# Kernel tuning notes

Measured on AMD Instinct MI355X. Metric: run time of the kernel, lower is better.

## Reference

```python
import jax, jax.numpy as jnp
import numpy as np
from jax import lax

STRIDE = 2  # down_sample_stride
MATMUL_NORM = True


def maxpool2d_5d(x, s):
    # x: [B, T, C, H, W]; kernel=s, stride=s, padding=(s-1)//2 == 0 for s=2
    return lax.reduce_window(
        x, -jnp.inf, lax.max,
        window_dimensions=(1, 1, 1, s, s),
        window_strides=(1, 1, 1, s, s),
        padding='VALID')


def setup_inputs() -> dict:
    key = jax.random.key(0)
    k1, k2, k3, k4 = jax.random.split(key, 4)
    B, T, Ck, Cv, H, W = 2, 4, 64, 256, 64, 64
    return {
        'memory_keys': jax.random.normal(k1, (B, T, Ck, H, W), jnp.float32),
        'memory_values': jax.random.normal(k2, (B, T, Cv, H, W), jnp.float32),
        'query_key': jax.random.normal(k3, (B, Ck, H, W), jnp.float32),
        'query_value': jax.random.normal(k4, (B, Cv, H, W), jnp.float32),
    }


def reference(memory_keys, memory_values, query_key, query_value):
    B, T, Ck, oH, oW = memory_keys.shape
    Cv = memory_values.shape[2]
    # down-sample memory bank (max pool, stride 2, no padding)
    mk = maxpool2d_5d(memory_keys, STRIDE)   # [B,T,Ck,h,w]
    mv = maxpool2d_5d(memory_values, STRIDE) # [B,T,Cv,h,w]
    h, w = mk.shape[-2], mk.shape[-1]
    M = T * h * w
    N = oH * oH  # code uses ori_height*ori_height (square assumed)
    # permute(0,2,1,3,4).view(B,Ck,M).permute(0,2,1) -> [B, M, Ck]
    mk = mk.transpose(0, 2, 1, 3, 4).reshape(B, Ck, M).transpose(0, 2, 1)
    qk = query_key.reshape(B, Ck, N)
    attn = jnp.einsum('bmc,bcn->bmn', mk, qk)  # [B, M, N]
    if MATMUL_NORM:
        attn = attn * (Ck ** -0.5)
    attn = jax.nn.softmax(attn, axis=1)  # softmax over memory positions
    mv = mv.transpose(0, 2, 1, 3, 4).reshape(B, Cv, M)
    memory = jnp.einsum('bcm,bmn->bcn', mv, attn).reshape(B, Cv, oH, oW)
    return jnp.concatenate([query_value, memory], axis=1)  # [B, 2*Cv, H, W]
```

## Files before the change

kernel.cpp:

```cpp
#include <hip/hip_runtime.h>
#include <hip/hip_bf16.h>
#include <math.h>

typedef unsigned short u16;
typedef unsigned int   u32;
typedef __attribute__((ext_vector_type(8))) short  bf16x8;
typedef __attribute__((ext_vector_type(4))) float  floatx4;

#define NB 2
#define NT 4
#define CK 64
#define CV 256
#define HH 64
#define WW 64
#define MM 4096
#define NN 4096
#define SCALE 0.125f
#define SHIFT 4.0f
#define OUT_B 2097152
#define NW 64
#define ITG 16
#define C1 0.18033688011112042f
#define C2 (-5.770780163555853f)

__device__ __forceinline__ u16 f2b(float f) {
    __hip_bfloat16 h = __float2bfloat16(f);
    union { __hip_bfloat16 h; u16 u; } v; v.h = h; return v.u;
}

#define PRE_K 65536
#define PRE_V 589824
#define PRE_T 1114112

__global__ void prep(const float* __restrict__ mk, const float* __restrict__ mv,
                     const float4* __restrict__ qv,
                     u16* __restrict__ pk2, u16* __restrict__ vt,
                     float* __restrict__ out) {
    int u = blockIdx.x * 256 + threadIdx.x;
    if (u < PRE_K) {
        int m = u & 4095, cb8 = (u >> 12) & 7, b = u >> 15;
        int t = m >> 10, hh = (m >> 5) & 31, ww = m & 31;
        const float* s0 = mk + ((size_t)((b*NT + t)*CK + cb8*8))*(HH*WW)
                             + (2*hh)*WW + 2*ww;
        bf16x8 fr;
        #pragma unroll
        for (int i = 0; i < 8; ++i) {
            const float* s = s0 + (size_t)i*(HH*WW);
            float2 r0 = *(const float2*)s;
            float2 r1 = *(const float2*)(s + WW);
            fr[i] = (short)f2b(fmaxf(fmaxf(r0.x, r0.y), fmaxf(r1.x, r1.y)));
        }
        *(bf16x8*)(pk2 + ((size_t)(b*8 + cb8)*MM + m)*8) = fr;
    } else if (u < PRE_V) {
        int u2 = u - PRE_K;
        int m4 = u2 & 1023, c = (u2 >> 10) & 255, b = u2 >> 18;
        int t = m4 >> 8, hh = (m4 >> 3) & 31, w8 = m4 & 7;
        const float* s0 = mv + ((size_t)((b*NT + t)*CV + c))*(HH*WW)
                             + (2*hh)*WW + 8*w8;
        float4 a0 = *(const float4*)(s0);
        float4 a1 = *(const float4*)(s0 + 4);
        float4 b0 = *(const float4*)(s0 + WW);
        float4 b1 = *(const float4*)(s0 + WW + 4);
        ushort4 r;
        r.x = f2b(fmaxf(fmaxf(a0.x, a0.y), fmaxf(b0.x, b0.y)));
        r.y = f2b(fmaxf(fmaxf(a0.z, a0.w), fmaxf(b0.z, b0.w)));
        r.z = f2b(fmaxf(fmaxf(a1.x, a1.y), fmaxf(b1.x, b1.y)));
        r.w = f2b(fmaxf(fmaxf(a1.z, a1.w), fmaxf(b1.z, b1.w)));
        *(ushort4*)(vt + ((size_t)(b*CV + c)*MM) + m4*4) = r;
    } else {
        int u3 = u - PRE_V;
        int b = u3 >> 18, ru = u3 & 262143;
        ((float4*)out)[(size_t)b*(OUT_B/4) + ru] = qv[u3];
    }
}

__device__ __forceinline__ void qk_phase(bf16x8 k0, bf16x8 k1,
        const bf16x8 (&qf)[2][4], float (&sacc)[4],
        u16* __restrict__ Pd, int lrow, int cbw, int sw)
{
    #pragma unroll
    for (int t = 0; t < 4; ++t) {
        floatx4 s = __builtin_amdgcn_mfma_f32_16x16x32_bf16(
                        k0, qf[0][t], (floatx4){0.f,0.f,0.f,0.f}, 0, 0, 0);
        s = __builtin_amdgcn_mfma_f32_16x16x32_bf16(k1, qf[1][t], s, 0, 0, 0);
        float p0 = exp2f(__builtin_fmaf(s[0], C1, C2));
        float p1 = exp2f(__builtin_fmaf(s[1], C1, C2));
        float p2 = exp2f(__builtin_fmaf(s[2], C1, C2));
        float p3 = exp2f(__builtin_fmaf(s[3], C1, C2));
        sacc[t] += (p0 + p1) + (p2 + p3);
        u32 d0 = (u32)f2b(p0) | ((u32)f2b(p1) << 16);
        u32 d1 = (u32)f2b(p2) | ((u32)f2b(p3) << 16);
        *(uint2*)&Pd[(t*16 + lrow)*128 + ((cbw ^ sw) << 2)] = make_uint2(d0, d1);
    }
}

__device__ __forceinline__ void pv_phase(const bf16x8 (&vf)[4],
        floatx4 (&oacc)[4], const u16* __restrict__ Ps,
        int lrow, int quad, int sw)
{
    #pragma unroll
    for (int cc = 0; cc < 4; ++cc) {
        bf16x8 pf[4];
        #pragma unroll
        for (int t = 0; t < 4; ++t) {
            int cb = (cc << 3) + (quad << 1);
            pf[t] = *(const bf16x8*)&Ps[(t*16 + lrow)*128 + ((cb ^ sw) << 2)];
        }
        __builtin_amdgcn_s_setprio(1);
        #pragma unroll
        for (int t = 0; t < 4; ++t)
            oacc[t] = __builtin_amdgcn_mfma_f32_16x16x32_bf16(
                          vf[cc], pf[t], oacc[t], 0, 0, 0);
        __builtin_amdgcn_s_setprio(0);
    }
}

__launch_bounds__(512, 4)
__global__ void attn_v8(const u16* __restrict__ pk2, const u16* __restrict__ vt,
                        const float* __restrict__ qk,
                        float* __restrict__ part, float* __restrict__ sums) {
    const int bid = blockIdx.x;
    const int xcd = bid & 7;
    const int b  = (xcd >> 2) & 1;
    const int cs = (xcd >> 1) & 1;
    const int ms = xcd & 1;
    const int ntile = bid >> 3;
    const int tid = threadIdx.x, w = tid >> 6, l = tid & 63;
    const int lrow = l & 15, quad = l >> 4;
    const int n0 = ntile * NW;
    const int sw  = lrow << 1;
    const int cbw = (w << 2) + quad;
    const int mstart = ms << 11;

    __shared__ __align__(16) u16 P[2][NW * 128];
    __shared__ float sums_s[8][NW];

    bf16x8 qf[2][4];
    const float* qb = qk + (size_t)b * CK * NN + n0;
    #pragma unroll
    for (int cc = 0; cc < 2; ++cc)
        #pragma unroll
        for (int t = 0; t < 4; ++t)
            #pragma unroll
            for (int i = 0; i < 8; ++i) {
                int c = cc*32 + quad*8 + i;
                qf[cc][t][i] = (short)f2b(qb[(size_t)c*NN + t*16 + lrow]);
            }

    const u16* pkb  = pk2 + (size_t)b * (8*MM*8);
    const int  mrw  = mstart + w*16 + lrow;
    const u16* vrow = vt + ((size_t)b*CV + cs*128 + w*16 + lrow)*MM
                         + mstart + quad*8;

    floatx4 oacc[4];
    #pragma unroll
    for (int t = 0; t < 4; ++t) oacc[t] = (floatx4){0.f, 0.f, 0.f, 0.f};
    float sacc[4] = {0.f, 0.f, 0.f, 0.f};

    bf16x8 k0 = *(const bf16x8*)(pkb + ((size_t)quad*MM + mrw)*8);
    bf16x8 k1 = *(const bf16x8*)(pkb + ((size_t)(quad+4)*MM + mrw)*8);
    bf16x8 vf[4];
    #pragma unroll
    for (int cc = 0; cc < 4; ++cc)
        vf[cc] = *(const bf16x8*)(vrow + cc*32);
    qk_phase(k0, k1, qf, sacc, P[0], lrow, cbw, sw);

    for (int it = 0; it < ITG - 1; ++it) {
        __syncthreads();
        const int mb2 = (it + 1) << 7;
        bf16x8 k0n = *(const bf16x8*)(pkb + ((size_t)quad*MM + mb2 + mrw)*8);
        bf16x8 k1n = *(const bf16x8*)(pkb + ((size_t)(quad+4)*MM + mb2 + mrw)*8);
        bf16x8 vn[4];
        #pragma unroll
        for (int cc = 0; cc < 4; ++cc)
            vn[cc] = *(const bf16x8*)(vrow + mb2 + cc*32);
        pv_phase(vf, oacc, P[it & 1], lrow, quad, sw);
        qk_phase(k0n, k1n, qf, sacc, P[(it + 1) & 1], lrow, cbw, sw);
        #pragma unroll
        for (int cc = 0; cc < 4; ++cc) vf[cc] = vn[cc];
    }
    __syncthreads();
    pv_phase(vf, oacc, P[(ITG - 1) & 1], lrow, quad, sw);

    #pragma unroll
    for (int t = 0; t < 4; ++t) {
        float v = sacc[t];
        v += __shfl_xor(v, 16, 64);
        v += __shfl_xor(v, 32, 64);
        if (l < 16) sums_s[w][t*16 + l] = v;
    }
    __syncthreads();

    float* pb = part + ((size_t)((((ms*NB + b)*2 + cs)*64) + ntile)) * (128*64);
    #pragma unroll
    for (int t = 0; t < 4; ++t)
        #pragma unroll
        for (int r = 0; r < 4; ++r) {
            int c_loc = w*16 + quad*4 + r;
            pb[c_loc*64 + t*16 + lrow] = oacc[t][r];
        }
    if (cs == 0 && tid < 64) {
        float sv = 0.f;
        #pragma unroll
        for (int w2 = 0; w2 < 8; ++w2) sv += sums_s[w2][tid];
        sums[((size_t)((ms*NB + b)*64 + ntile))*64 + tid] = sv;
    }
}

__global__ void epilogue2(const float* __restrict__ part,
                          const float* __restrict__ sums,
                          float* __restrict__ out) {
    int e = blockIdx.x * 256 + threadIdx.x;
    int nl4 = e & 15;
    int nt  = (e >> 4) & 63;
    int c   = (e >> 10) & 255;
    int b   = e >> 18;
    int cs = c >> 7, cl = c & 127;
    const float4* p4 = (const float4*)part;
    const float4* s4 = (const float4*)sums;
    size_t t0 = (size_t)(((0*NB + b)*2 + cs)*64 + nt);
    size_t t1 = (size_t)(((1*NB + b)*2 + cs)*64 + nt);
    float4 u0 = p4[t0*2048 + cl*16 + nl4];
    float4 u1 = p4[t1*2048 + cl*16 + nl4];
    float4 d0 = s4[((size_t)((0*NB + b)*64 + nt))*16 + nl4];
    float4 d1 = s4[((size_t)((1*NB + b)*64 + nt))*16 + nl4];
    float4 r;
    r.x = (u0.x + u1.x) / (d0.x + d1.x);
    r.y = (u0.y + u1.y) / (d0.y + d1.y);
    r.z = (u0.z + u1.z) / (d0.z + d1.z);
    r.w = (u0.w + u1.w) / (d0.w + d1.w);
    ((float4*)out)[(size_t)(b*512 + 256 + c)*1024 + nt*16 + nl4] = r;
}


__global__ void pool_v_f32(const float* __restrict__ src, float* __restrict__ out) {
    int e = blockIdx.x * 256 + threadIdx.x;
    int c = e & 255;
    int r = e >> 8;
    int ww = r & 31;  int hh = (r >> 5) & 31;
    int t  = (r >> 10) & 3;  int b = r >> 12;
    int m  = r & (MM - 1);
    const float* s = src + ((size_t)(((b*NT + t)*CV + c)*HH + 2*hh))*WW + 2*ww;
    out[(size_t)b*OUT_B + (size_t)m*CV + c] = fmaxf(fmaxf(s[0], s[1]), fmaxf(s[WW], s[WW+1]));
}

__global__ void pool_k_f32(const float* __restrict__ src, float* __restrict__ dst) {
    int e = blockIdx.x * 256 + threadIdx.x;
    int c = e & 63;
    int r = e >> 6;
    int ww = r & 31;  int hh = (r >> 5) & 31;
    int t  = (r >> 10) & 3;  int b = r >> 12;
    const float* s = src + ((size_t)(((b*NT + t)*CK + c)*HH + 2*hh))*WW + 2*ww;
    dst[e] = fmaxf(fmaxf(s[0], s[1]), fmaxf(s[WW], s[WW+1]));
}

__global__ void copy_qv_f32(const float4* __restrict__ src, float4* __restrict__ dst) {
    int u = blockIdx.x * 256 + threadIdx.x;
    int b  = u >> 18;
    int ru = u & 262143;
    dst[(size_t)b * (OUT_B/4) + ru] = src[u];
}

template<bool STAGED_K>
__launch_bounds__(256)
__global__ void attn_old(const float* __restrict__ pk,
                         const float* __restrict__ mk,
                         const float* __restrict__ qk,
                         float* __restrict__ out) {
    __shared__ __align__(16) float q_lds[CK][4];
    __shared__ __align__(16) float sarr[4][MM];
    __shared__ float inv_l[4];

    const int tid = threadIdx.x;
    const int blk = blockIdx.x;
    const int b   = blk >> 10;
    const int n0  = (blk & 1023) << 2;

    {
        int c = tid >> 2, qi = tid & 3;
        q_lds[c][qi] = qk[((size_t)(b*CK + c))*NN + n0 + qi];
    }
    __syncthreads();

    #pragma unroll
    for (int i = 0; i < 16; ++i) {
        int m = tid + (i << 8);
        float a0 = 0.f, a1 = 0.f, a2 = 0.f, a3 = 0.f;
        if (STAGED_K) {
            const float4* k4 = reinterpret_cast<const float4*>(pk + ((size_t)b*MM + m)*CK);
            #pragma unroll
            for (int cc = 0; cc < 16; ++cc) {
                float4 kv = k4[cc];
                int c = cc*4;
                float4 q0 = *reinterpret_cast<const float4*>(&q_lds[c][0]);
                float4 q1 = *reinterpret_cast<const float4*>(&q_lds[c+1][0]);
                float4 q2 = *reinterpret_cast<const float4*>(&q_lds[c+2][0]);
                float4 q3 = *reinterpret_cast<const float4*>(&q_lds[c+3][0]);
                a0 += kv.x*q0.x + kv.y*q1.x + kv.z*q2.x + kv.w*q3.x;
                a1 += kv.x*q0.y + kv.y*q1.y + kv.z*q2.y + kv.w*q3.y;
                a2 += kv.x*q0.z + kv.y*q1.z + kv.z*q2.z + kv.w*q3.z;
                a3 += kv.x*q0.w + kv.y*q1.w + kv.z*q2.w + kv.w*q3.w;
            }
        } else {
            int ww = m & 31, hh = (m >> 5) & 31, t = m >> 10;
            const float* base = mk + ((size_t)((b*NT + t)*CK)*HH + 2*hh)*WW + 2*ww;
            for (int c = 0; c < CK; ++c) {
                const float* s = base + (size_t)c*HH*WW;
                float kv = fmaxf(fmaxf(s[0], s[1]), fmaxf(s[WW], s[WW+1]));
                float4 q = *reinterpret_cast<const float4*>(&q_lds[c][0]);
                a0 += kv*q.x; a1 += kv*q.y; a2 += kv*q.z; a3 += kv*q.w;
            }
        }
        sarr[0][m] = a0*SCALE;
        sarr[1][m] = a1*SCALE;
        sarr[2][m] = a2*SCALE;
        sarr[3][m] = a3*SCALE;
    }
    __syncthreads();

    const int wave = tid >> 6, lane = tid & 63;
    float mx = -3.0e38f;
    for (int m = lane; m < MM; m += 64) mx = fmaxf(mx, sarr[wave][m]);
    #pragma unroll
    for (int off = 32; off > 0; off >>= 1) mx = fmaxf(mx, __shfl_xor(mx, off, 64));
    float ls = 0.f;
    for (int m = lane; m < MM; m += 64) {
        float p = __expf(sarr[wave][m] - mx);
        sarr[wave][m] = p;
        ls += p;
    }
    #pragma unroll
    for (int off = 32; off > 0; off >>= 1) ls += __shfl_xor(ls, off, 64);
    if (lane == 0) inv_l[wave] = 1.0f / ls;
    __syncthreads();

    const int c4 = lane;
    const float4* vb = reinterpret_cast<const float4*>(out + (size_t)b*OUT_B) + c4;
    const float* prow = sarr[wave];
    float a0 = 0.f, a1 = 0.f, a2 = 0.f, a3 = 0.f;
    for (int m = 0; m < MM; m += 4) {
        float4 p4 = *reinterpret_cast<const float4*>(prow + m);
        const float4* vp = vb + (size_t)m*(CV/4);
        float4 v0 = vp[0], v1 = vp[CV/4], v2 = vp[CV/2], v3 = vp[3*(CV/4)];
        a0 += p4.x*v0.x + p4.y*v1.x + p4.z*v2.x + p4.w*v3.x;
        a1 += p4.x*v0.y + p4.y*v1.y + p4.z*v2.y + p4.w*v3.y;
        a2 += p4.x*v0.z + p4.y*v1.z + p4.z*v2.z + p4.w*v3.z;
        a3 += p4.x*v0.w + p4.y*v1.w + p4.z*v2.w + p4.w*v3.w;
    }

    float inv = inv_l[wave];
    int n = n0 + wave;
    size_t ob = ((size_t)(b*512 + 256 + c4*4))*NN + n;
    out[ob]        = a0*inv;
    out[ob + NN]   = a1*inv;
    out[ob + 2*NN] = a2*inv;
    out[ob + 3*NN] = a3*inv;
}


extern "C" void kernel_launch(void* const* d_in, const int* in_sizes, int n_in,
                              void* d_out, int out_size, void* d_ws, size_t ws_size,
                              hipStream_t stream) {
    const float* mk = (const float*)d_in[0];
    const float* mv = (const float*)d_in[1];
    const float* qk = (const float*)d_in[2];
    const float* qv = (const float*)d_in[3];
    float* out = (float*)d_out;

    u16* pk2 = (u16*)d_ws;
    u16* vt  = pk2 + (size_t)NB*8*MM*8;
    float* part = (float*)(vt + (size_t)NB*CV*MM);
    float* sums = part + 4194304;
    const size_t need = ((size_t)NB*8*MM*8 + (size_t)NB*CV*MM) * sizeof(u16)
                      + (4194304 + 16384) * sizeof(float);

    if (ws_size >= need) {
        prep<<<PRE_T/256, 256, 0, stream>>>(mk, mv, (const float4*)qv, pk2, vt, out);
        attn_v8<<<512, 512, 0, stream>>>(pk2, vt, qk, part, sums);
        epilogue2<<<524288/256, 256, 0, stream>>>(part, sums, out);
    } else {
        const size_t pk_bytes = (size_t)NB*MM*CK*sizeof(float);
        const bool staged = (ws_size >= pk_bytes);
        float* pk = (float*)d_ws;
        pool_v_f32<<<(NB*MM*CV)/256, 256, 0, stream>>>(mv, out);
        if (staged) {
            pool_k_f32<<<(NB*MM*CK)/256, 256, 0, stream>>>(mk, pk);
            attn_old<true ><<<NB*(NN/4), 256, 0, stream>>>(pk, mk, qk, out);
        } else {
            attn_old<false><<<NB*(NN/4), 256, 0, stream>>>(pk, mk, qk, out);
        }
        copy_qv_f32<<<((NB*CV*HH*WW)/4)/256, 256, 0, stream>>>((const float4*)qv, (float4*)out);
    }
}
```

Baseline: 143.4 us.

## Merge Cv halves per block so QK softmax is computed once, use raw exp/cvt asm

Each block now covers all 256 value channels (two 16-row tiles per wave) instead of splitting Cv into two halves across blocks. This stops the QK^T scores and exponentials from being computed twice, and the grid shrinks from 512 to 256 blocks. The exp2 call and the bf16 packing are replaced with inline v_exp_f32 and v_cvt_pk_bf16_f32 to cut VALU work. The trade-offs are higher register pressure (launch bounds drop to 2 blocks per CU) and fewer blocks for occupancy.

```diff
diff --git a/kernel.cpp b/kernel.cpp
--- a/kernel.cpp
+++ b/kernel.cpp
@@ -26,6 +26,17 @@
 __device__ __forceinline__ u16 f2b(float f) {
     __hip_bfloat16 h = __float2bfloat16(f);
     union { __hip_bfloat16 h; u16 u; } v; v.h = h; return v.u;
+}
+
+__device__ __forceinline__ float fexp2(float x) {
+    float r;
+    asm("v_exp_f32 %0, %1" : "=v"(r) : "v"(x));
+    return r;
+}
+__device__ __forceinline__ u32 cvtpk_bf16(float a, float b) {
+    u32 r;
+    asm("v_cvt_pk_bf16_f32 %0, %1, %2" : "=v"(r) : "v"(a), "v"(b));
+    return r;
 }
 
 #define PRE_K 65536
@@ -83,48 +94,46 @@
         floatx4 s = __builtin_amdgcn_mfma_f32_16x16x32_bf16(
                         k0, qf[0][t], (floatx4){0.f,0.f,0.f,0.f}, 0, 0, 0);
         s = __builtin_amdgcn_mfma_f32_16x16x32_bf16(k1, qf[1][t], s, 0, 0, 0);
-        float p0 = exp2f(__builtin_fmaf(s[0], C1, C2));
-        float p1 = exp2f(__builtin_fmaf(s[1], C1, C2));
-        float p2 = exp2f(__builtin_fmaf(s[2], C1, C2));
-        float p3 = exp2f(__builtin_fmaf(s[3], C1, C2));
+        float p0 = fexp2(__builtin_fmaf(s[0], C1, C2));
+        float p1 = fexp2(__builtin_fmaf(s[1], C1, C2));
+        float p2 = fexp2(__builtin_fmaf(s[2], C1, C2));
+        float p3 = fexp2(__builtin_fmaf(s[3], C1, C2));
         sacc[t] += (p0 + p1) + (p2 + p3);
-        u32 d0 = (u32)f2b(p0) | ((u32)f2b(p1) << 16);
-        u32 d1 = (u32)f2b(p2) | ((u32)f2b(p3) << 16);
+        u32 d0 = cvtpk_bf16(p0, p1);
+        u32 d1 = cvtpk_bf16(p2, p3);
         *(uint2*)&Pd[(t*16 + lrow)*128 + ((cbw ^ sw) << 2)] = make_uint2(d0, d1);
     }
 }
 
-__device__ __forceinline__ void pv_phase(const bf16x8 (&vf)[4],
-        floatx4 (&oacc)[4], const u16* __restrict__ Ps,
+__device__ __forceinline__ void pv_phase(const bf16x8 (&vf)[4][2],
+        floatx4 (&oacc)[2][4], const u16* __restrict__ Ps,
         int lrow, int quad, int sw)
 {
     #pragma unroll
-    for (int cc = 0; cc < 4; ++cc) {
-        bf16x8 pf[4];
-        #pragma unroll
-        for (int t = 0; t < 4; ++t) {
-            int cb = (cc << 3) + (quad << 1);
-            pf[t] = *(const bf16x8*)&Ps[(t*16 + lrow)*128 + ((cb ^ sw) << 2)];
+    for (int kt = 0; kt < 4; ++kt) {
+        int cb = (kt << 3) + (quad << 1);
+        #pragma unroll
+        for (int nt = 0; nt < 4; ++nt) {
+            bf16x8 pf = *(const bf16x8*)&Ps[(nt*16 + lrow)*128 + ((cb ^ sw) << 2)];
+            __builtin_amdgcn_s_setprio(1);
+            oacc[0][nt] = __builtin_amdgcn_mfma_f32_16x16x32_bf16(
+                              vf[kt][0], pf, oacc[0][nt], 0, 0, 0);
+            oacc[1][nt] = __builtin_amdgcn_mfma_f32_16x16x32_bf16(
+                              vf[kt][1], pf, oacc[1][nt], 0, 0, 0);
+            __builtin_amdgcn_s_setprio(0);
         }
-        __builtin_amdgcn_s_setprio(1);
-        #pragma unroll
-        for (int t = 0; t < 4; ++t)
-            oacc[t] = __builtin_amdgcn_mfma_f32_16x16x32_bf16(
-                          vf[cc], pf[t], oacc[t], 0, 0, 0);
-        __builtin_amdgcn_s_setprio(0);
-    }
-}
-
-__launch_bounds__(512, 4)
-__global__ void attn_v8(const u16* __restrict__ pk2, const u16* __restrict__ vt,
-                        const float* __restrict__ qk,
-                        float* __restrict__ part, float* __restrict__ sums) {
+    }
+}
+
+__launch_bounds__(512, 2)
+__global__ void attn_v10(const u16* __restrict__ pk2, const u16* __restrict__ vt,
+                         const float* __restrict__ qk,
+                         float* __restrict__ part, float* __restrict__ sums) {
     const int bid = blockIdx.x;
-    const int xcd = bid & 7;
-    const int b  = (xcd >> 2) & 1;
-    const int cs = (xcd >> 1) & 1;
-    const int ms = xcd & 1;
-    const int ntile = bid >> 3;
+    const int xcd = bid & 7, grp = bid >> 3;
+    const int b   = (xcd >> 2) & 1;
+    const int ms  = xcd & 1;
+    const int ntile = (((xcd >> 1) & 1) << 5) | grp;
     const int tid = threadIdx.x, w = tid >> 6, l = tid & 63;
     const int lrow = l & 15, quad = l >> 4;
     const int n0 = ntile * NW;
@@ -149,20 +158,24 @@
 
     const u16* pkb  = pk2 + (size_t)b * (8*MM*8);
     const int  mrw  = mstart + w*16 + lrow;
-    const u16* vrow = vt + ((size_t)b*CV + cs*128 + w*16 + lrow)*MM
-                         + mstart + quad*8;
-
-    floatx4 oacc[4];
-    #pragma unroll
-    for (int t = 0; t < 4; ++t) oacc[t] = (floatx4){0.f, 0.f, 0.f, 0.f};
+    const u16* vrow = vt + ((size_t)b*CV + w*32 + lrow)*MM + mstart + quad*8;
+
+    floatx4 oacc[2][4];
+    #pragma unroll
+    for (int j = 0; j < 2; ++j)
+        #pragma unroll
+        for (int nt = 0; nt < 4; ++nt)
+            oacc[j][nt] = (floatx4){0.f, 0.f, 0.f, 0.f};
     float sacc[4] = {0.f, 0.f, 0.f, 0.f};
 
     bf16x8 k0 = *(const bf16x8*)(pkb + ((size_t)quad*MM + mrw)*8);
     bf16x8 k1 = *(const bf16x8*)(pkb + ((size_t)(quad+4)*MM + mrw)*8);
-    bf16x8 vf[4];
-    #pragma unroll
-    for (int cc = 0; cc < 4; ++cc)
-        vf[cc] = *(const bf16x8*)(vrow + cc*32);
+    bf16x8 vf[4][2];
+    #pragma unroll
+    for (int kt = 0; kt < 4; ++kt)
+        #pragma unroll
+        for (int j = 0; j < 2; ++j)
+            vf[kt][j] = *(const bf16x8*)(vrow + (size_t)j*(16*MM) + kt*32);
     qk_phase(k0, k1, qf, sacc, P[0], lrow, cbw, sw);
 
     for (int it = 0; it < ITG - 1; ++it) {
@@ -170,14 +183,19 @@
         const int mb2 = (it + 1) << 7;
         bf16x8 k0n = *(const bf16x8*)(pkb + ((size_t)quad*MM + mb2 + mrw)*8);
         bf16x8 k1n = *(const bf16x8*)(pkb + ((size_t)(quad+4)*MM + mb2 + mrw)*8);
-        bf16x8 vn[4];
-        #pragma unroll
-        for (int cc = 0; cc < 4; ++cc)
-            vn[cc] = *(const bf16x8*)(vrow + mb2 + cc*32);
+        bf16x8 vn[4][2];
+        #pragma unroll
+        for (int kt = 0; kt < 4; ++kt)
+            #pragma unroll
+            for (int j = 0; j < 2; ++j)
+                vn[kt][j] = *(const bf16x8*)(vrow + (size_t)j*(16*MM) + mb2 + kt*32);
         pv_phase(vf, oacc, P[it & 1], lrow, quad, sw);
         qk_phase(k0n, k1n, qf, sacc, P[(it + 1) & 1], lrow, cbw, sw);
         #pragma unroll
-        for (int cc = 0; cc < 4; ++cc) vf[cc] = vn[cc];
+        for (int kt = 0; kt < 4; ++kt)
+            #pragma unroll
+            for (int j = 0; j < 2; ++j)
+                vf[kt][j] = vn[kt][j];
     }
     __syncthreads();
     pv_phase(vf, oacc, P[(ITG - 1) & 1], lrow, quad, sw);
@@ -191,15 +209,17 @@
     }
     __syncthreads();
 
-    float* pb = part + ((size_t)((((ms*NB + b)*2 + cs)*64) + ntile)) * (128*64);
-    #pragma unroll
-    for (int t = 0; t < 4; ++t)
-        #pragma unroll
-        for (int r = 0; r < 4; ++r) {
-            int c_loc = w*16 + quad*4 + r;
-            pb[c_loc*64 + t*16 + lrow] = oacc[t][r];
-        }
-    if (cs == 0 && tid < 64) {
+    float* pb = part + ((size_t)((ms*NB + b)*64 + ntile)) * (256*64);
+    #pragma unroll
+    for (int j = 0; j < 2; ++j)
+        #pragma unroll
+        for (int nt = 0; nt < 4; ++nt)
+            #pragma unroll
+            for (int r = 0; r < 4; ++r) {
+                int c_loc = w*32 + j*16 + quad*4 + r;
+                pb[c_loc*64 + nt*16 + lrow] = oacc[j][nt][r];
+            }
+    if (tid < 64) {
         float sv = 0.f;
         #pragma unroll
         for (int w2 = 0; w2 < 8; ++w2) sv += sums_s[w2][tid];
@@ -207,7 +227,7 @@
     }
 }
 
-__global__ void epilogue2(const float* __restrict__ part,
+__global__ void epilogue3(const float* __restrict__ part,
                           const float* __restrict__ sums,
                           float* __restrict__ out) {
     int e = blockIdx.x * 256 + threadIdx.x;
@@ -215,15 +235,14 @@
     int nt  = (e >> 4) & 63;
     int c   = (e >> 10) & 255;
     int b   = e >> 18;
-    int cs = c >> 7, cl = c & 127;
     const float4* p4 = (const float4*)part;
     const float4* s4 = (const float4*)sums;
-    size_t t0 = (size_t)(((0*NB + b)*2 + cs)*64 + nt);
-    size_t t1 = (size_t)(((1*NB + b)*2 + cs)*64 + nt);
-    float4 u0 = p4[t0*2048 + cl*16 + nl4];
-    float4 u1 = p4[t1*2048 + cl*16 + nl4];
-    float4 d0 = s4[((size_t)((0*NB + b)*64 + nt))*16 + nl4];
-    float4 d1 = s4[((size_t)((1*NB + b)*64 + nt))*16 + nl4];
+    size_t t0 = (size_t)((0*NB + b)*64 + nt);
+    size_t t1 = (size_t)((1*NB + b)*64 + nt);
+    float4 u0 = p4[t0*4096 + c*16 + nl4];
+    float4 u1 = p4[t1*4096 + c*16 + nl4];
+    float4 d0 = s4[t0*16 + nl4];
+    float4 d1 = s4[t1*16 + nl4];
     float4 r;
     r.x = (u0.x + u1.x) / (d0.x + d1.x);
     r.y = (u0.y + u1.y) / (d0.y + d1.y);
@@ -376,8 +395,8 @@
 
     if (ws_size >= need) {
         prep<<<PRE_T/256, 256, 0, stream>>>(mk, mv, (const float4*)qv, pk2, vt, out);
-        attn_v8<<<512, 512, 0, stream>>>(pk2, vt, qk, part, sums);
-        epilogue2<<<524288/256, 256, 0, stream>>>(part, sums, out);
+        attn_v10<<<256, 512, 0, stream>>>(pk2, vt, qk, part, sums);
+        epilogue3<<<524288/256, 256, 0, stream>>>(part, sums, out);
     } else {
         const size_t pk_bytes = (size_t)NB*MM*CK*sizeof(float);
         const bool staged = (ws_size >= pk_bytes);
```

Measured after the change: 140.2 us. 1.02x faster.
